# Kernel tuning notes

Hardware: AMD Instinct MI355X
Metric: run time of the kernel (lower is better)

## Reference

```python
import jax, jax.numpy as jnp
import numpy as np

THRESHOLD = 0.5
NEG_POS = 3
ALPHA = 1.0


def cxcy_to_xy(b):
    return jnp.concatenate([b[:, :2] - b[:, 2:] / 2, b[:, :2] + b[:, 2:] / 2], axis=-1)


def xy_to_cxcy(b):
    return jnp.concatenate([(b[:, :2] + b[:, 2:]) / 2, b[:, 2:] - b[:, :2]], axis=-1)


def encode_bboxes(cxcy, priors_cxcy):
    # standard SSD encoding with variances (0.1, 0.2)
    g_cxcy = (cxcy[:, :2] - priors_cxcy[:, :2]) / (priors_cxcy[:, 2:] / 10.0)
    g_wh = jnp.log(cxcy[:, 2:] / priors_cxcy[:, 2:]) * 5.0
    return jnp.concatenate([g_cxcy, g_wh], axis=-1)


def compute_iou(a, b):
    # a: [n,4] xyxy, b: [m,4] xyxy -> [n,m]
    lt = jnp.maximum(a[:, None, :2], b[None, :, :2])
    rb = jnp.minimum(a[:, None, 2:], b[None, :, 2:])
    wh = jnp.clip(rb - lt, 0.0)
    inter = wh[..., 0] * wh[..., 1]
    area_a = (a[:, 2] - a[:, 0]) * (a[:, 3] - a[:, 1])
    area_b = (b[:, 2] - b[:, 0]) * (b[:, 3] - b[:, 1])
    return inter / (area_a[:, None] + area_b[None, :] - inter)


def setup_inputs() -> dict:
    key = jax.random.key(0)
    k1, k2, k3, k4, k5, k6 = jax.random.split(key, 6)
    B, D, C, O = 128, 8732, 21, 16
    loc_pred = jax.random.normal(k1, (B, D, 4), dtype=jnp.float32)
    cls_pred = jax.random.normal(k2, (B, D, C), dtype=jnp.float32)
    # valid gt boxes: xmin<xmax, ymin<ymax
    p = jax.random.uniform(k3, (B, O, 4), dtype=jnp.float32)
    x1 = jnp.minimum(p[..., 0], p[..., 2])
    x2 = jnp.maximum(p[..., 0], p[..., 2]) + 1e-2
    y1 = jnp.minimum(p[..., 1], p[..., 3])
    y2 = jnp.maximum(p[..., 1], p[..., 3]) + 1e-2
    gt_boxes = jnp.stack([x1, y1, x2, y2], axis=-1)
    gt_labels = jax.random.randint(k4, (B, O), 1, C)
    # priors in cxcywh, w/h in (0.05, 0.5)
    cxy = jax.random.uniform(k5, (D, 2), dtype=jnp.float32)
    wh = jax.random.uniform(k6, (D, 2), dtype=jnp.float32) * 0.45 + 0.05
    default_boxes = jnp.concatenate([cxy, wh], axis=-1)
    return {"loc_pred": loc_pred, "cls_pred": cls_pred, "gt_boxes": gt_boxes,
            "gt_labels": gt_labels, "default_boxes": default_boxes}


def _match_and_losses(loc_pred, cls_pred, gt_boxes, gt_labels, default_boxes):
    B, D, C = cls_pred.shape
    O = gt_boxes.shape[1]
    db_xy = cxcy_to_xy(default_boxes)

    def match_one(boxes_i, labels_i):
        iou = compute_iou(boxes_i, db_xy)                 # [O, D]
        best_truth_overlap = iou.max(axis=0)              # [D]
        best_truth_idx = iou.argmax(axis=0)               # [D]
        best_default_idx = iou.argmax(axis=1)             # [O]
        best_truth_idx = best_truth_idx.at[best_default_idx].set(jnp.arange(O))
        best_truth_overlap = best_truth_overlap.at[best_default_idx].set(1.0)
        labels = labels_i[best_truth_idx]                 # [D]
        labels = jnp.where(best_truth_overlap < THRESHOLD, 0, labels)
        matched_xy = boxes_i[best_truth_idx]              # [D,4]
        loc = encode_bboxes(xy_to_cxcy(matched_xy), default_boxes)
        return loc, labels

    loc_t, conf_t = jax.vmap(match_one)(gt_boxes, gt_labels)  # [B,D,4], [B,D]
    loc_t = jax.lax.stop_gradient(loc_t)  # targets carry no grad (requires_grad=False)

    pos = conf_t > 0                                      # [B,D]
    n_positive = pos.sum(axis=1)                          # [B]
    n_pos_total = n_positive.sum()

    # SmoothL1 (beta=1), mean over positive elements (num_pos * 4)
    diff = loc_pred - loc_t
    ad = jnp.abs(diff)
    sl1 = jnp.where(ad < 1.0, 0.5 * diff * diff, ad - 0.5)
    loc_loss = (sl1 * pos[..., None]).sum() / (n_pos_total.astype(jnp.float32) * 4.0)

    # per-element cross entropy
    logp = jax.nn.log_softmax(cls_pred, axis=-1)          # [B,D,C]
    ce = -jnp.take_along_axis(logp, conf_t[..., None], axis=-1)[..., 0]  # [B,D]

    conf_pos_sum = (ce * pos).sum()
    neg_loss = jnp.where(pos, 0.0, ce)
    neg_sorted = -jnp.sort(-neg_loss, axis=1)             # descending per row
    ranks = jnp.arange(D)[None, :]
    hard = ranks < (NEG_POS * n_positive)[:, None]
    conf_neg_sum = (neg_sorted * hard).sum()
    conf_loss = (conf_neg_sum + conf_pos_sum) / n_pos_total.astype(jnp.float32)

    return ALPHA * loc_loss + conf_loss


def reference(loc_pred, cls_pred, gt_boxes, gt_labels, default_boxes):
    return _match_and_losses(loc_pred, cls_pred, gt_boxes, gt_labels, default_boxes)
```

## Files before the change

kernel.cpp:

```cpp
#include <hip/hip_runtime.h>

#define BB 128
#define DD 8732
#define OO 16
#define CC 21
#define NG4 2183
#define NBLK_C 9
#define NLB (BB * NBLK_C)
#define NV 35

__device__ __forceinline__ float smoothl1(float d) {
    float ad = fabsf(d);
    return (ad < 1.0f) ? 0.5f * d * d : ad - 0.5f;
}

__global__ __launch_bounds__(256) void fused_all(
    const float4* __restrict__ loc_pred,
    const float*  __restrict__ cls,
    const float4* __restrict__ gt_boxes,
    const int*    __restrict__ gt_labels,
    const float4* __restrict__ db,
    unsigned long long* __restrict__ partial,
    float* __restrict__ ce_neg,
    float* __restrict__ part_sl1,
    int*   __restrict__ part_np,
    float* __restrict__ part_ce)
{
    const int b = blockIdx.y, jb = blockIdx.x, tid = threadIdx.x;
    const int g = jb * 256 + tid;
    __shared__ float s_ax1[OO], s_ay1[OO], s_ax2[OO], s_ay2[OO], s_area[OO];
    __shared__ int   s_lab[OO];
    __shared__ unsigned long long s_keys[8][257];
    __shared__ float s_f[8];
    __shared__ int   s_i[4];

    if (tid < OO) {
        float4 gg = gt_boxes[b * OO + tid];
        s_ax1[tid] = gg.x; s_ay1[tid] = gg.y; s_ax2[tid] = gg.z; s_ay2[tid] = gg.w;
        s_area[tid] = (gg.z - gg.x) * (gg.w - gg.y);
        s_lab[tid] = gt_labels[b * OO + tid];
    }
    __syncthreads();

    unsigned long long key[OO];
    #pragma unroll
    for (int o = 0; o < OO; ++o) key[o] = 0ull;
    int lab_r[4] = {0, 0, 0, 0};
    int bi_r[4]  = {0, 0, 0, 0};

    const int row0 = g * 4;
    if (g < NG4) {
        #pragma unroll
        for (int r = 0; r < 4; ++r) {
            const int d = row0 + r;
            float4 p = db[d];
            float px1 = p.x - p.z * 0.5f, py1 = p.y - p.w * 0.5f;
            float px2 = p.x + p.z * 0.5f, py2 = p.y + p.w * 0.5f;
            float area_b = (px2 - px1) * (py2 - py1);
            unsigned dl = (unsigned)(DD - 1 - d);
            float best = -1.0f; int bi = 0;
            #pragma unroll
            for (int o = 0; o < OO; ++o) {
                float w = fmaxf(fminf(s_ax2[o], px2) - fmaxf(s_ax1[o], px1), 0.0f);
                float h = fmaxf(fminf(s_ay2[o], py2) - fmaxf(s_ay1[o], py1), 0.0f);
                float inter = w * h;
                float uni = s_area[o] + area_b - inter;
                float iou = inter * __builtin_amdgcn_rcpf(uni);
                unsigned long long kk = ((unsigned long long)__float_as_uint(iou) << 32) | dl;
                if (kk > key[o]) key[o] = kk;
                if (iou > best) { best = iou; bi = o; }
            }
            lab_r[r] = (best < 0.5f) ? 0 : s_lab[bi];
            bi_r[r]  = bi;
        }
    }

    #pragma unroll
    for (int o = 0; o < 8; ++o) s_keys[o][tid] = key[o];
    __syncthreads();
    if (tid < 128) {
        const int o = tid >> 4, j = tid & 15;
        unsigned long long mx = s_keys[o][j];
        #pragma unroll
        for (int m = 1; m < 16; ++m) {
            unsigned long long v = s_keys[o][j + 16 * m];
            if (v > mx) mx = v;
        }
        #pragma unroll
        for (int off = 8; off; off >>= 1) {
            unsigned long long v = __shfl_xor(mx, off, 16);
            if (v > mx) mx = v;
        }
        if (j == 0) atomicMax(&partial[b * OO + o], mx);
    }
    __syncthreads();
    #pragma unroll
    for (int o = 0; o < 8; ++o) s_keys[o][tid] = key[8 + o];
    __syncthreads();
    if (tid < 128) {
        const int o = tid >> 4, j = tid & 15;
        unsigned long long mx = s_keys[o][j];
        #pragma unroll
        for (int m = 1; m < 16; ++m) {
            unsigned long long v = s_keys[o][j + 16 * m];
            if (v > mx) mx = v;
        }
        #pragma unroll
        for (int off = 8; off; off >>= 1) {
            unsigned long long v = __shfl_xor(mx, off, 16);
            if (v > mx) mx = v;
        }
        if (j == 0) atomicMax(&partial[b * OO + 8 + o], mx);
    }

    float sl1 = 0.0f, cepos = 0.0f; int npos = 0;
    if (g < NG4) {
        const size_t gi4 = (size_t)b * DD + row0;
        float e[84];
        const float4* src = (const float4*)(cls + gi4 * CC);
        #pragma unroll
        for (int jv = 0; jv < 21; ++jv) {
            float4 q = src[jv];
            e[4*jv+0] = q.x; e[4*jv+1] = q.y; e[4*jv+2] = q.z; e[4*jv+3] = q.w;
        }
        float out[4];
        #pragma unroll
        for (int r = 0; r < 4; ++r) {
            const int lab = lab_r[r];
            float m = e[21*r];
            #pragma unroll
            for (int c = 1; c < CC; ++c) m = fmaxf(m, e[21*r + c]);
            float s = 0.0f;
            #pragma unroll
            for (int c = 0; c < CC; ++c) s += __expf(e[21*r + c] - m);
            float xl = (lab == 0) ? e[21*r] : cls[(gi4 + r) * CC + lab];
            float ce = m + __logf(s) - xl;
            if (lab > 0) {
                npos += 1; cepos += ce;
                const int bi = bi_r[r];
                float ax1 = s_ax1[bi], ay1 = s_ay1[bi], ax2 = s_ax2[bi], ay2 = s_ay2[bi];
                float cx = (ax1 + ax2) * 0.5f, cy = (ay1 + ay2) * 0.5f;
                float w = ax2 - ax1, h = ay2 - ay1;
                float4 p = db[row0 + r];
                float gx = (cx - p.x) / (p.z / 10.0f);
                float gy = (cy - p.y) / (p.w / 10.0f);
                float gw = __logf(w / p.z) * 5.0f;
                float gh = __logf(h / p.w) * 5.0f;
                float4 lp = loc_pred[gi4 + r];
                sl1 += smoothl1(lp.x - gx) + smoothl1(lp.y - gy)
                     + smoothl1(lp.z - gw) + smoothl1(lp.w - gh);
                out[r] = 0.0f;
            } else {
                out[r] = ce;
            }
        }
        *(float4*)(ce_neg + gi4) = make_float4(out[0], out[1], out[2], out[3]);
    }

    #pragma unroll
    for (int off = 32; off; off >>= 1) {
        sl1   += __shfl_xor(sl1, off);
        cepos += __shfl_xor(cepos, off);
        npos  += __shfl_xor(npos, off);
    }
    const int w = tid >> 6;
    if ((tid & 63) == 0) { s_f[w*2+0] = sl1; s_f[w*2+1] = cepos; s_i[w] = npos; }
    __syncthreads();
    if (tid == 0) {
        float sv = 0, cp = 0; int np = 0;
        #pragma unroll
        for (int q = 0; q < 4; ++q) { sv += s_f[q*2+0]; cp += s_f[q*2+1]; np += s_i[q]; }
        const int pi = b * NBLK_C + jb;
        part_sl1[pi] = sv;
        part_ce[pi]  = cp;
        part_np[pi]  = np;
    }
}

__global__ __launch_bounds__(256) void topk_final(
    const float*  __restrict__ cls,
    const float4* __restrict__ loc_pred,
    const float4* __restrict__ gt_boxes,
    const int*    __restrict__ gt_labels,
    const float4* __restrict__ db,
    const unsigned long long* __restrict__ partial,
    float* __restrict__ ce_neg,
    const float* __restrict__ part_sl1,
    const int*   __restrict__ part_np,
    const float* __restrict__ part_ce,
    float* __restrict__ img_sl1,
    float* __restrict__ img_ce,
    int*   __restrict__ img_np,
    float* __restrict__ conf_neg_part,
    int*   __restrict__ done_counter,
    float* __restrict__ out)
{
    const int b = blockIdx.x, tid = threadIdx.x;
    __shared__ int      hist[256];
    __shared__ unsigned s_pk[2];
    __shared__ float    s_f[12];
    __shared__ int      s_c[4];
    __shared__ int      s_bdi[OO], s_lab[OO];
    __shared__ float    s_ax1[OO], s_ay1[OO], s_ax2[OO], s_ay2[OO], s_area[OO];
    __shared__ float    s_dsl1, s_dce;
    __shared__ int      s_dnp, s_np;
    __shared__ float    s_isl1, s_ice;
    __shared__ int      s_last;

    if (tid < OO) {
        float4 gg = gt_boxes[b * OO + tid];
        s_ax1[tid] = gg.x; s_ay1[tid] = gg.y; s_ax2[tid] = gg.z; s_ay2[tid] = gg.w;
        s_area[tid] = (gg.z - gg.x) * (gg.w - gg.y);
        s_lab[tid] = gt_labels[b * OO + tid];
        s_bdi[tid] = DD - 1 - (int)(partial[b * OO + tid] & 0xffffffffu);
    }
    __syncthreads();

    float dsl1 = 0.0f, dce = 0.0f; int dnp = 0;
    if (tid < OO) {
        const int R = s_bdi[tid];
        bool winner = true;
        for (int o2 = tid + 1; o2 < OO; ++o2)
            if (s_bdi[o2] == R) winner = false;
        if (winner) {
            float4 p = db[R];
            float px1 = p.x - p.z * 0.5f, py1 = p.y - p.w * 0.5f;
            float px2 = p.x + p.z * 0.5f, py2 = p.y + p.w * 0.5f;
            float area_b = (px2 - px1) * (py2 - py1);
            float best = -1.0f; int bi = 0;
            #pragma unroll
            for (int o = 0; o < OO; ++o) {
                float w = fmaxf(fminf(s_ax2[o], px2) - fmaxf(s_ax1[o], px1), 0.0f);
                float h = fmaxf(fminf(s_ay2[o], py2) - fmaxf(s_ay1[o], py1), 0.0f);
                float inter = w * h;
                float uni = s_area[o] + area_b - inter;
                float iou = inter * __builtin_amdgcn_rcpf(uni);
                if (iou > best) { best = iou; bi = o; }
            }
            int lab0 = (best < 0.5f) ? 0 : s_lab[bi];

            const float* x = cls + ((size_t)b * DD + R) * CC;
            float m = x[0];
            #pragma unroll
            for (int c = 1; c < CC; ++c) m = fmaxf(m, x[c]);
            float s = 0.0f;
            #pragma unroll
            for (int c = 0; c < CC; ++c) s += __expf(x[c] - m);
            float lse = m + __logf(s);
            float4 lp = loc_pred[(size_t)b * DD + R];

            if (lab0 > 0) {
                dce -= (lse - x[lab0]);
                dnp -= 1;
                float ax1 = s_ax1[bi], ay1 = s_ay1[bi], ax2 = s_ax2[bi], ay2 = s_ay2[bi];
                float cx = (ax1 + ax2) * 0.5f, cy = (ay1 + ay2) * 0.5f;
                float w = ax2 - ax1, h = ay2 - ay1;
                float gx = (cx - p.x) / (p.z / 10.0f);
                float gy = (cy - p.y) / (p.w / 10.0f);
                float gw = __logf(w / p.z) * 5.0f;
                float gh = __logf(h / p.w) * 5.0f;
                dsl1 -= smoothl1(lp.x - gx) + smoothl1(lp.y - gy)
                      + smoothl1(lp.z - gw) + smoothl1(lp.w - gh);
            } else {
                ce_neg[(size_t)b * DD + R] = 0.0f;
            }
            dce += (lse - x[s_lab[tid]]);
            dnp += 1;
            {
                float ax1 = s_ax1[tid], ay1 = s_ay1[tid], ax2 = s_ax2[tid], ay2 = s_ay2[tid];
                float cx = (ax1 + ax2) * 0.5f, cy = (ay1 + ay2) * 0.5f;
                float w = ax2 - ax1, h = ay2 - ay1;
                float gx = (cx - p.x) / (p.z / 10.0f);
                float gy = (cy - p.y) / (p.w / 10.0f);
                float gw = __logf(w / p.z) * 5.0f;
                float gh = __logf(h / p.w) * 5.0f;
                dsl1 += smoothl1(lp.x - gx) + smoothl1(lp.y - gy)
                      + smoothl1(lp.z - gw) + smoothl1(lp.w - gh);
            }
        }
    }
    if (tid < 64) {
        #pragma unroll
        for (int off = 8; off; off >>= 1) {
            dsl1 += __shfl_xor(dsl1, off, 16);
            dce  += __shfl_xor(dce, off, 16);
            dnp  += __shfl_xor(dnp, off, 16);
        }
        if (tid == 0) { s_dsl1 = dsl1; s_dce = dce; s_dnp = dnp; }
    }
    __syncthreads();

    if (tid == 0) {
        float a = 0, c2 = 0; int n = 0;
        #pragma unroll
        for (int j = 0; j < NBLK_C; ++j) {
            a  += part_sl1[b * NBLK_C + j];
            c2 += part_ce[b * NBLK_C + j];
            n  += part_np[b * NBLK_C + j];
        }
        s_isl1 = a + s_dsl1; s_ice = c2 + s_dce; s_np = n + s_dnp;
    }
    __syncthreads();

    int k0 = 3 * s_np;
    if (k0 > DD) k0 = DD;

    float row = 0.0f;
    if (k0 > 0) {
        unsigned kx[NV];
        #pragma unroll
        for (int q = 0; q < NV; ++q) {
            int d = q * 256 + tid;
            float v = (d < DD) ? ce_neg[(size_t)b * DD + d] : 0.0f;
            unsigned u = __float_as_uint(v);
            kx[q] = u ^ ((unsigned)((int)u >> 31) | 0x80000000u);
        }
        unsigned prefix = 0u; int k = k0;
        #pragma unroll
        for (int p = 0; p < 4; ++p) {
            const int shift = 24 - 8 * p;
            hist[tid] = 0;
            __syncthreads();
            #pragma unroll
            for (int q = 0; q < NV; ++q) {
                if (p == 0 || ((kx[q] ^ prefix) >> (shift + 8)) == 0u)
                    atomicAdd(&hist[(kx[q] >> shift) & 255], 1);
            }
            __syncthreads();
            if (tid < 64) {
                int h0 = hist[255 - 4*tid], h1 = hist[254 - 4*tid],
                    h2 = hist[253 - 4*tid], h3 = hist[252 - 4*tid];
                int sl = h0 + h1 + h2 + h3;
                int run = sl;
                #pragma unroll
                for (int off = 1; off < 64; off <<= 1) {
                    int v = __shfl_up(run, off);
                    if (tid >= off) run += v;
                }
                int pre = run - sl;
                if (pre < k && k <= pre + sl) {
                    int hh[4] = {h0, h1, h2, h3};
                    int c = pre, byte = -1, knew = 0;
                    #pragma unroll
                    for (int j = 0; j < 4; ++j) {
                        if (byte < 0 && c + hh[j] >= k) { byte = 255 - 4*tid - j; knew = k - c; }
                        c += hh[j];
                    }
                    s_pk[0] = prefix | ((unsigned)byte << shift);
                    s_pk[1] = (unsigned)knew;
                }
            }
            __syncthreads();
            prefix = s_pk[0]; k = (int)s_pk[1];
        }
        unsigned vb = (prefix & 0x80000000u) ? (prefix ^ 0x80000000u) : ~prefix;
        float vk = __uint_as_float(vb);

        float ssum = 0.0f; int cgt = 0;
        #pragma unroll
        for (int q = 0; q < NV; ++q) {
            if (kx[q] > prefix) {
                unsigned u = (kx[q] & 0x80000000u) ? (kx[q] ^ 0x80000000u) : ~kx[q];
                ssum += __uint_as_float(u);
                ++cgt;
            }
        }
        #pragma unroll
        for (int off = 32; off; off >>= 1) { ssum += __shfl_xor(ssum, off); cgt += __shfl_xor(cgt, off); }
        if ((tid & 63) == 0) { s_f[tid >> 6] = ssum; s_c[tid >> 6] = cgt; }
        __syncthreads();
        row = s_f[0]+s_f[1]+s_f[2]+s_f[3]
            + (float)(k0 - (s_c[0]+s_c[1]+s_c[2]+s_c[3])) * vk;
    }

    if (tid == 0) {
        conf_neg_part[b] = row;
        img_sl1[b] = s_isl1; img_ce[b] = s_ice; img_np[b] = s_np;
        __threadfence();
        int prev = atomicAdd(done_counter, 1);
        s_last = (prev == BB - 1) ? 1 : 0;
    }
    __syncthreads();
    if (s_last) {
        __threadfence();
        float loc = 0.0f, cp = 0.0f, cn = 0.0f; int npt = 0;
        if (tid < BB) {
            loc = img_sl1[tid]; cp = img_ce[tid];
            cn = conf_neg_part[tid]; npt = img_np[tid];
        }
        #pragma unroll
        for (int off = 32; off; off >>= 1) {
            loc += __shfl_xor(loc, off);
            cp  += __shfl_xor(cp, off);
            cn  += __shfl_xor(cn, off);
            npt += __shfl_xor(npt, off);
        }
        const int w = tid >> 6;
        if ((tid & 63) == 0) { s_f[w*3+0] = loc; s_f[w*3+1] = cp; s_f[w*3+2] = cn; s_c[w] = npt; }
        __syncthreads();
        if (tid == 0) {
            float L = 0, P = 0, N = 0; int T = 0;
            #pragma unroll
            for (int q = 0; q < 4; ++q) { L += s_f[q*3]; P += s_f[q*3+1]; N += s_f[q*3+2]; T += s_c[q]; }
            float npf = (float)T;
            out[0] = L / (npf * 4.0f) + (N + P) / npf;
        }
    }
}

extern "C" void kernel_launch(void* const* d_in, const int* in_sizes, int n_in,
                              void* d_out, int out_size, void* d_ws, size_t ws_size,
                              hipStream_t stream) {
    (void)in_sizes; (void)n_in; (void)out_size; (void)ws_size;
    const float4* loc_pred  = (const float4*)d_in[0];
    const float*  cls_pred  = (const float*)d_in[1];
    const float4* gt_boxes  = (const float4*)d_in[2];
    const int*    gt_labels = (const int*)d_in[3];
    const float4* db        = (const float4*)d_in[4];

    char* ws = (char*)d_ws;
    size_t off = 0;
    auto alloc = [&](size_t bytes) { char* p = ws + off; off = (off + bytes + 15) & ~(size_t)15; return p; };

    unsigned long long* partial = (unsigned long long*)alloc((size_t)BB * OO * 8);
    int*   done_counter  = (int*)alloc(16);
    float* ce_neg        = (float*)alloc((size_t)BB * DD * 4);
    float* part_sl1      = (float*)alloc((size_t)NLB * 4);
    int*   part_np       = (int*)alloc((size_t)NLB * 4);
    float* part_ce       = (float*)alloc((size_t)NLB * 4);
    float* img_sl1       = (float*)alloc((size_t)BB * 4);
    float* img_ce        = (float*)alloc((size_t)BB * 4);
    int*   img_np        = (int*)alloc((size_t)BB * 4);
    float* conf_neg_part = (float*)alloc((size_t)BB * 4);

    hipMemsetAsync(partial, 0, (size_t)BB * OO * 8 + 16, stream);

    fused_all<<<dim3(NBLK_C, BB), 256, 0, stream>>>(loc_pred, cls_pred, gt_boxes,
                                                    gt_labels, db, partial,
                                                    ce_neg, part_sl1, part_np, part_ce);
    topk_final<<<BB, 256, 0, stream>>>(cls_pred, loc_pred, gt_boxes, gt_labels, db,
                                       partial, ce_neg, part_sl1, part_np, part_ce,
                                       img_sl1, img_ce, img_np, conf_neg_part,
                                       done_counter, (float*)d_out);
}
```

Baseline: 67.39 us.

## Process one prior per thread and stage class logits in LDS via direct loads

Each thread now handles one default box instead of four, so the grid grows from 9 to 35 blocks per batch image. Each block's class-logit tile is copied into shared memory with the hardware global-to-LDS load path instead of being held in an 84-float register array. The per-object max-IoU key reduction now uses wave shuffles plus a small cross-wave step, replacing the larger shared-memory staging. The aim is more parallelism and latency hiding on a memory-bound load, and lower register pressure, at the cost of about 21 KB of LDS per block and more blocks issuing atomics.

```diff
diff --git a/kernel.cpp b/kernel.cpp
--- a/kernel.cpp
+++ b/kernel.cpp
@@ -4,10 +4,12 @@
 #define DD 8732
 #define OO 16
 #define CC 21
-#define NG4 2183
-#define NBLK_C 9
+#define NBLK_C 35
 #define NLB (BB * NBLK_C)
 #define NV 35
+
+typedef __attribute__((address_space(3))) unsigned int lds_u32;
+typedef const __attribute__((address_space(1))) unsigned int glb_u32;
 
 __device__ __forceinline__ float smoothl1(float d) {
     float ad = fabsf(d);
@@ -27,10 +29,11 @@
     float* __restrict__ part_ce)
 {
     const int b = blockIdx.y, jb = blockIdx.x, tid = threadIdx.x;
-    const int g = jb * 256 + tid;
+    const int d = jb * 256 + tid;
+    __shared__ float s_cls[256 * CC];
     __shared__ float s_ax1[OO], s_ay1[OO], s_ax2[OO], s_ay2[OO], s_area[OO];
     __shared__ int   s_lab[OO];
-    __shared__ unsigned long long s_keys[8][257];
+    __shared__ unsigned long long swave[4][OO];
     __shared__ float s_f[8];
     __shared__ int   s_i[4];
 
@@ -42,119 +45,99 @@
     }
     __syncthreads();
 
+    const int nrow = min(256, DD - jb * 256);
+    const int nvec = nrow * CC / 4;
+    const float4* src = (const float4*)(cls + ((size_t)b * DD + (size_t)jb * 256) * CC);
+    if (nvec == 1344) {
+        #pragma unroll
+        for (int c = 0; c < 5; ++c) {
+            int v = c * 256 + tid;
+            __builtin_amdgcn_global_load_lds((glb_u32*)(src + v),
+                                             (lds_u32*)&s_cls[v * 4], 16, 0, 0);
+        }
+        if (tid < 64) {
+            int v = 5 * 256 + tid;
+            __builtin_amdgcn_global_load_lds((glb_u32*)(src + v),
+                                             (lds_u32*)&s_cls[v * 4], 16, 0, 0);
+        }
+    } else {
+        for (int v = tid; v < nvec; v += 256)
+            __builtin_amdgcn_global_load_lds((glb_u32*)(src + v),
+                                             (lds_u32*)&s_cls[v * 4], 16, 0, 0);
+    }
+
     unsigned long long key[OO];
     #pragma unroll
     for (int o = 0; o < OO; ++o) key[o] = 0ull;
-    int lab_r[4] = {0, 0, 0, 0};
-    int bi_r[4]  = {0, 0, 0, 0};
-
-    const int row0 = g * 4;
-    if (g < NG4) {
-        #pragma unroll
-        for (int r = 0; r < 4; ++r) {
-            const int d = row0 + r;
+    int lab = 0, bi = 0;
+    if (d < DD) {
+        float4 p = db[d];
+        float px1 = p.x - p.z * 0.5f, py1 = p.y - p.w * 0.5f;
+        float px2 = p.x + p.z * 0.5f, py2 = p.y + p.w * 0.5f;
+        float area_b = (px2 - px1) * (py2 - py1);
+        unsigned dl = (unsigned)(DD - 1 - d);
+        float best = -1.0f;
+        #pragma unroll
+        for (int o = 0; o < OO; ++o) {
+            float w = fmaxf(fminf(s_ax2[o], px2) - fmaxf(s_ax1[o], px1), 0.0f);
+            float h = fmaxf(fminf(s_ay2[o], py2) - fmaxf(s_ay1[o], py1), 0.0f);
+            float inter = w * h;
+            float uni = s_area[o] + area_b - inter;
+            float iou = inter * __builtin_amdgcn_rcpf(uni);
+            unsigned long long kk = ((unsigned long long)__float_as_uint(iou) << 32) | dl;
+            if (kk > key[o]) key[o] = kk;
+            if (iou > best) { best = iou; bi = o; }
+        }
+        lab = (best < 0.5f) ? 0 : s_lab[bi];
+    }
+
+    #pragma unroll
+    for (int o = 0; o < OO; ++o) {
+        unsigned long long k = key[o];
+        #pragma unroll
+        for (int off = 32; off; off >>= 1) {
+            unsigned long long v = __shfl_xor(k, off);
+            if (v > k) k = v;
+        }
+        if ((tid & 63) == 0) swave[tid >> 6][o] = k;
+    }
+
+    __syncthreads();
+
+    if (tid < OO) {
+        unsigned long long m = swave[0][tid];
+        #pragma unroll
+        for (int w = 1; w < 4; ++w) if (swave[w][tid] > m) m = swave[w][tid];
+        atomicMax(&partial[b * OO + tid], m);
+    }
+
+    float sl1 = 0.0f, cepos = 0.0f; int npos = 0;
+    if (d < DD) {
+        const size_t gi = (size_t)b * DD + d;
+        float m = s_cls[tid * CC];
+        #pragma unroll
+        for (int c = 1; c < CC; ++c) m = fmaxf(m, s_cls[tid * CC + c]);
+        float s = 0.0f;
+        #pragma unroll
+        for (int c = 0; c < CC; ++c) s += __expf(s_cls[tid * CC + c] - m);
+        float xl = s_cls[tid * CC + lab];
+        float ce = m + __logf(s) - xl;
+
+        if (lab > 0) {
+            npos = 1; cepos = ce;
+            float ax1 = s_ax1[bi], ay1 = s_ay1[bi], ax2 = s_ax2[bi], ay2 = s_ay2[bi];
+            float cx = (ax1 + ax2) * 0.5f, cy = (ay1 + ay2) * 0.5f;
+            float w = ax2 - ax1, h = ay2 - ay1;
             float4 p = db[d];
-            float px1 = p.x - p.z * 0.5f, py1 = p.y - p.w * 0.5f;
-            float px2 = p.x + p.z * 0.5f, py2 = p.y + p.w * 0.5f;
-            float area_b = (px2 - px1) * (py2 - py1);
-            unsigned dl = (unsigned)(DD - 1 - d);
-            float best = -1.0f; int bi = 0;
-            #pragma unroll
-            for (int o = 0; o < OO; ++o) {
-                float w = fmaxf(fminf(s_ax2[o], px2) - fmaxf(s_ax1[o], px1), 0.0f);
-                float h = fmaxf(fminf(s_ay2[o], py2) - fmaxf(s_ay1[o], py1), 0.0f);
-                float inter = w * h;
-                float uni = s_area[o] + area_b - inter;
-                float iou = inter * __builtin_amdgcn_rcpf(uni);
-                unsigned long long kk = ((unsigned long long)__float_as_uint(iou) << 32) | dl;
-                if (kk > key[o]) key[o] = kk;
-                if (iou > best) { best = iou; bi = o; }
-            }
-            lab_r[r] = (best < 0.5f) ? 0 : s_lab[bi];
-            bi_r[r]  = bi;
-        }
-    }
-
-    #pragma unroll
-    for (int o = 0; o < 8; ++o) s_keys[o][tid] = key[o];
-    __syncthreads();
-    if (tid < 128) {
-        const int o = tid >> 4, j = tid & 15;
-        unsigned long long mx = s_keys[o][j];
-        #pragma unroll
-        for (int m = 1; m < 16; ++m) {
-            unsigned long long v = s_keys[o][j + 16 * m];
-            if (v > mx) mx = v;
-        }
-        #pragma unroll
-        for (int off = 8; off; off >>= 1) {
-            unsigned long long v = __shfl_xor(mx, off, 16);
-            if (v > mx) mx = v;
-        }
-        if (j == 0) atomicMax(&partial[b * OO + o], mx);
-    }
-    __syncthreads();
-    #pragma unroll
-    for (int o = 0; o < 8; ++o) s_keys[o][tid] = key[8 + o];
-    __syncthreads();
-    if (tid < 128) {
-        const int o = tid >> 4, j = tid & 15;
-        unsigned long long mx = s_keys[o][j];
-        #pragma unroll
-        for (int m = 1; m < 16; ++m) {
-            unsigned long long v = s_keys[o][j + 16 * m];
-            if (v > mx) mx = v;
-        }
-        #pragma unroll
-        for (int off = 8; off; off >>= 1) {
-            unsigned long long v = __shfl_xor(mx, off, 16);
-            if (v > mx) mx = v;
-        }
-        if (j == 0) atomicMax(&partial[b * OO + 8 + o], mx);
-    }
-
-    float sl1 = 0.0f, cepos = 0.0f; int npos = 0;
-    if (g < NG4) {
-        const size_t gi4 = (size_t)b * DD + row0;
-        float e[84];
-        const float4* src = (const float4*)(cls + gi4 * CC);
-        #pragma unroll
-        for (int jv = 0; jv < 21; ++jv) {
-            float4 q = src[jv];
-            e[4*jv+0] = q.x; e[4*jv+1] = q.y; e[4*jv+2] = q.z; e[4*jv+3] = q.w;
-        }
-        float out[4];
-        #pragma unroll
-        for (int r = 0; r < 4; ++r) {
-            const int lab = lab_r[r];
-            float m = e[21*r];
-            #pragma unroll
-            for (int c = 1; c < CC; ++c) m = fmaxf(m, e[21*r + c]);
-            float s = 0.0f;
-            #pragma unroll
-            for (int c = 0; c < CC; ++c) s += __expf(e[21*r + c] - m);
-            float xl = (lab == 0) ? e[21*r] : cls[(gi4 + r) * CC + lab];
-            float ce = m + __logf(s) - xl;
-            if (lab > 0) {
-                npos += 1; cepos += ce;
-                const int bi = bi_r[r];
-                float ax1 = s_ax1[bi], ay1 = s_ay1[bi], ax2 = s_ax2[bi], ay2 = s_ay2[bi];
-                float cx = (ax1 + ax2) * 0.5f, cy = (ay1 + ay2) * 0.5f;
-                float w = ax2 - ax1, h = ay2 - ay1;
-                float4 p = db[row0 + r];
-                float gx = (cx - p.x) / (p.z / 10.0f);
-                float gy = (cy - p.y) / (p.w / 10.0f);
-                float gw = __logf(w / p.z) * 5.0f;
-                float gh = __logf(h / p.w) * 5.0f;
-                float4 lp = loc_pred[gi4 + r];
-                sl1 += smoothl1(lp.x - gx) + smoothl1(lp.y - gy)
-                     + smoothl1(lp.z - gw) + smoothl1(lp.w - gh);
-                out[r] = 0.0f;
-            } else {
-                out[r] = ce;
-            }
-        }
-        *(float4*)(ce_neg + gi4) = make_float4(out[0], out[1], out[2], out[3]);
+            float gx = (cx - p.x) / (p.z / 10.0f);
+            float gy = (cy - p.y) / (p.w / 10.0f);
+            float gw = __logf(w / p.z) * 5.0f;
+            float gh = __logf(h / p.w) * 5.0f;
+            float4 lp = loc_pred[gi];
+            sl1 = smoothl1(lp.x - gx) + smoothl1(lp.y - gy)
+                + smoothl1(lp.z - gw) + smoothl1(lp.w - gh);
+        }
+        ce_neg[gi] = (lab > 0) ? 0.0f : ce;
     }
 
     #pragma unroll
```

Measured after the change: 87.40 us. 1.3x slower.
